# Performance work log

Hardware: AMD Instinct MI355X
Metric: run time of the kernel (lower is better)

The kernel has to match this reference:

```python
import jax, jax.numpy as jnp
import numpy as np

S_LEN, B, H, V, L = 128, 128, 1024, 32000, 2
H2 = 512  # ceil(H/2)
WSZ = 10
MAXW = 2 * WSZ + 1


def setup_inputs() -> dict:
    key = jax.random.key(0)
    k = jax.random.split(key, 16)
    def n(ki, shape, s=0.02):
        return jax.random.normal(ki, shape, dtype=jnp.float32) * s
    return {
        "source_sentence_length": S_LEN,
        "encoder_output": jax.random.normal(k[0], (S_LEN, B, H), dtype=jnp.float32),
        "word": jax.random.randint(k[1], (1, B), 0, V),
        "h0": jax.random.normal(k[2], (L, B, H), dtype=jnp.float32),
        "c0": jax.random.normal(k[3], (L, B, H), dtype=jnp.float32),
        "embedding": n(k[4], (V, H)),
        "lstm_Wih": n(k[5], (L, 4 * H, H)),
        "lstm_Whh": n(k[6], (L, 4 * H, H)),
        "lstm_bih": jnp.zeros((L, 4 * H), jnp.float32),
        "lstm_bhh": jnp.zeros((L, 4 * H), jnp.float32),
        "attn_w1": n(k[7], (H2, H)),
        "attn_b1": jnp.zeros((H2,), jnp.float32),
        "attn_w2": n(k[8], (1, H2)),
        "attn_b2": jnp.zeros((1,), jnp.float32),
        "fc1_w": n(k[9], (H, 2 * H)),
        "fc1_b": jnp.zeros((H,), jnp.float32),
        "fc2_w": n(k[10], (V, H)),
        "fc2_b": jnp.zeros((V,), jnp.float32),
    }


def reference(source_sentence_length, encoder_output, word, h0, c0, embedding,
              lstm_Wih, lstm_Whh, lstm_bih, lstm_bhh,
              attn_w1, attn_b1, attn_w2, attn_b2,
              fc1_w, fc1_b, fc2_w, fc2_b):
    S = source_sentence_length
    std2 = (WSZ / 2.0) ** 2  # std_squared from the module

    # embedding lookup: word [1,B] -> [1,B,H]; single-step multi-layer LSTM
    x = embedding[word][0]  # [B,H]
    hs, cs = [], []
    for l in range(h0.shape[0]):
        gates = x @ lstm_Wih[l].T + lstm_bih[l] + h0[l] @ lstm_Whh[l].T + lstm_bhh[l]
        i, f, g, o = jnp.split(gates, 4, axis=-1)
        c = jax.nn.sigmoid(f) * c0[l] + jax.nn.sigmoid(i) * jnp.tanh(g)
        h = jax.nn.sigmoid(o) * jnp.tanh(c)
        hs.append(h); cs.append(c); x = h
    h_new = jnp.stack(hs)
    c_new = jnp.stack(cs)
    out = x[None]  # decoder output [1,B,H]

    # predicted window center p in [0,S]
    p = S * jax.nn.sigmoid(jnp.tanh(out @ attn_w1.T + attn_b1) @ attn_w2.T + attn_b2)
    pb = p[0, :, 0]  # [B]
    ws = jnp.round(jnp.clip(pb - WSZ, 0, None)).astype(jnp.int32)
    we = jnp.round(jnp.clip(pb + WSZ, None, S - 1)).astype(jnp.int32)

    # windowed gather: position j of window b is source index ws[b]+j
    idx = ws[:, None] + jnp.arange(MAXW, dtype=jnp.int32)  # [B,MAXW]
    valid = idx <= we[:, None]
    enc_b = encoder_output.transpose(1, 0, 2)  # [B,S,H]
    h_s = jnp.take_along_axis(enc_b, jnp.clip(idx, 0, S - 1)[:, :, None], axis=1)
    h_s = jnp.where(valid[:, :, None], h_s, 0.0)  # zero-padded as in the torch code

    # faithful (non-negative, non-squared) gaussian term: exp((pos - p)/(2*std^2))
    gauss = jnp.where(valid, jnp.exp((idx.astype(enc_b.dtype) - pb[:, None]) / (2.0 * std2)), 0.0)

    scores = jnp.einsum('bh,bwh->bw', out[0], h_s)  # zero-padded slots score 0, kept in softmax
    a = jax.nn.softmax(scores, axis=-1) * gauss  # [B,MAXW]
    ctx = jnp.einsum('bw,bwh->bh', a, h_s)[None]  # [1,B,H]

    cat = jnp.concatenate([ctx, out], axis=2)  # [1,B,2H]
    o2 = jnp.tanh(cat @ fc1_w.T + fc1_b)
    y = jax.nn.log_softmax(o2 @ fc2_w.T + fc2_b, axis=2)  # [1,B,V]
    return (y, o2, h_new, c_new, a)
```

## Files before the change

### kernel.cpp

```cpp
#include <hip/hip_runtime.h>
#include <math.h>

namespace {

constexpr int B    = 128;
constexpr int H    = 1024;
constexpr int V    = 32000;
constexpr int WSZ  = 10;
constexpr int MAXW = 2 * WSZ + 1;

typedef __attribute__((ext_vector_type(8))) short bf16x8;
typedef __attribute__((ext_vector_type(4))) short short4v;
typedef __attribute__((ext_vector_type(4))) float f32x4;

__device__ __forceinline__ float sigf(float x) { return 1.0f / (1.0f + expf(-x)); }

__device__ __forceinline__ unsigned short rnebf(float f) {
    unsigned u = __float_as_uint(f);
    u += 0x7fffu + ((u >> 16) & 1u);
    return (unsigned short)(u >> 16);
}

__device__ __forceinline__ bf16x8 cvt8(const f32x4 a, const f32x4 b) {
    bf16x8 r;
    r[0] = (short)rnebf(a.x); r[1] = (short)rnebf(a.y);
    r[2] = (short)rnebf(a.z); r[3] = (short)rnebf(a.w);
    r[4] = (short)rnebf(b.x); r[5] = (short)rnebf(b.y);
    r[6] = (short)rnebf(b.z); r[7] = (short)rnebf(b.w);
    return r;
}

__device__ __forceinline__ void gl_lds16(const float* g, float* l) {
    __builtin_amdgcn_global_load_lds(
        (const __attribute__((address_space(1))) unsigned int*)g,
        (__attribute__((address_space(3))) unsigned int*)l,
        16, 0, 0);
}

struct S3 { short h, m, l; };

__device__ __forceinline__ S3 split3(float x) {
    S3 r;
    const unsigned uh = __float_as_uint(x) & 0xFFFF0000u;
    const float fh = __uint_as_float(uh);
    const float r1 = x - fh;
    const unsigned um = __float_as_uint(r1) & 0xFFFF0000u;
    const float fm = __uint_as_float(um);
    const float r2 = r1 - fm;
    const unsigned ul = __float_as_uint(r2) & 0xFFFF0000u;
    r.h = (short)(uh >> 16);
    r.m = (short)(um >> 16);
    r.l = (short)(ul >> 16);
    return r;
}

__device__ __forceinline__ void split8(const f32x4 a, const f32x4 b,
                                       bf16x8& wh, bf16x8& wm, bf16x8& wl) {
    S3 s;
    s = split3(a.x); wh[0] = s.h; wm[0] = s.m; wl[0] = s.l;
    s = split3(a.y); wh[1] = s.h; wm[1] = s.m; wl[1] = s.l;
    s = split3(a.z); wh[2] = s.h; wm[2] = s.m; wl[2] = s.l;
    s = split3(a.w); wh[3] = s.h; wm[3] = s.m; wl[3] = s.l;
    s = split3(b.x); wh[4] = s.h; wm[4] = s.m; wl[4] = s.l;
    s = split3(b.y); wh[5] = s.h; wm[5] = s.m; wl[5] = s.l;
    s = split3(b.z); wh[6] = s.h; wm[6] = s.m; wl[6] = s.l;
    s = split3(b.w); wh[7] = s.h; wm[7] = s.m; wl[7] = s.l;
}

__global__ __launch_bounds__(256, 2) void lstm_gemm(
    const short* __restrict__ Ah0, const short* __restrict__ Am0, const short* __restrict__ Al0,
    const short* __restrict__ Ah1, const short* __restrict__ Am1, const short* __restrict__ Al1,
    const float* __restrict__ W0, const float* __restrict__ W1,
    float* __restrict__ outbase)
{
    __shared__ float wt[2][4160];

    const int t    = threadIdx.x;
    const int lane = t & 63;
    const int w    = t >> 6;
    const int m16  = lane & 15;
    const int g    = lane >> 4;
    const int n0   = blockIdx.x * 64;
    const int y    = blockIdx.y;
    const int src  = y >> 2;
    const int k0   = (y & 3) * 256;
    const short* Ah = src ? Ah1 : Ah0;
    const short* Am = src ? Am1 : Am0;
    const short* Al = src ? Al1 : Al0;
    const float* W  = src ? W1  : W0;
    float* out = outbase + (size_t)y * 128 * 4096;

    bf16x8 ah[2][8], am[2][8], al[2][8];
    #pragma unroll
    for (int q = 0; q < 2; ++q) {
        const size_t ao = (size_t)((w * 2 + q) * 16 + m16) * 1024 + k0 + g * 8;
        #pragma unroll
        for (int s = 0; s < 8; ++s) {
            ah[q][s] = *(const bf16x8*)(Ah + ao + s * 32);
            am[q][s] = *(const bf16x8*)(Am + ao + s * 32);
            al[q][s] = *(const bf16x8*)(Al + ao + s * 32);
        }
    }

#define LSTM_STAGE(BUF, C)                                                  \
    {                                                                       \
        _Pragma("unroll")                                                   \
        for (int i = 0; i < 5; ++i) {                                       \
            const int idx = i * 256 + t;                                    \
            const int rr  = idx / 65;                                       \
            const int pp  = idx - rr * 65;                                  \
            if (idx < 1040 && pp < 64) {                                    \
                const float* s_ = W + (size_t)(n0 + (C) * 16 + rr) * 1024   \
                                + k0 + pp * 4;                              \
                gl_lds16(s_, &wt[BUF][(size_t)(i * 256 + w * 64) * 4]);     \
            }                                                               \
        }                                                                   \
    }

    LSTM_STAGE(0, 0)
    int cur = 0;
    #pragma unroll
    for (int c = 0; c < 4; ++c) {
        __syncthreads();
        if (c < 3) {
            if (cur == 0) LSTM_STAGE(1, c + 1)
            else          LSTM_STAGE(0, c + 1)
        }
        f32x4 acc0 = {}, acc1 = {};
        const float* lrow = &wt[cur][m16 * 260 + g * 8];
        #pragma unroll
        for (int s = 0; s < 8; ++s) {
            const f32x4 wa = *(const f32x4*)(lrow + s * 32);
            const f32x4 wb = *(const f32x4*)(lrow + s * 32 + 4);
            bf16x8 wh, wm, wl;
            split8(wa, wb, wh, wm, wl);
            acc0 = __builtin_amdgcn_mfma_f32_16x16x32_bf16(ah[0][s], wh, acc0, 0, 0, 0);
            acc0 = __builtin_amdgcn_mfma_f32_16x16x32_bf16(ah[0][s], wm, acc0, 0, 0, 0);
            acc0 = __builtin_amdgcn_mfma_f32_16x16x32_bf16(am[0][s], wh, acc0, 0, 0, 0);
            acc0 = __builtin_amdgcn_mfma_f32_16x16x32_bf16(ah[0][s], wl, acc0, 0, 0, 0);
            acc0 = __builtin_amdgcn_mfma_f32_16x16x32_bf16(am[0][s], wm, acc0, 0, 0, 0);
            acc0 = __builtin_amdgcn_mfma_f32_16x16x32_bf16(al[0][s], wh, acc0, 0, 0, 0);
            acc1 = __builtin_amdgcn_mfma_f32_16x16x32_bf16(ah[1][s], wh, acc1, 0, 0, 0);
            acc1 = __builtin_amdgcn_mfma_f32_16x16x32_bf16(ah[1][s], wm, acc1, 0, 0, 0);
            acc1 = __builtin_amdgcn_mfma_f32_16x16x32_bf16(am[1][s], wh, acc1, 0, 0, 0);
            acc1 = __builtin_amdgcn_mfma_f32_16x16x32_bf16(ah[1][s], wl, acc1, 0, 0, 0);
            acc1 = __builtin_amdgcn_mfma_f32_16x16x32_bf16(am[1][s], wm, acc1, 0, 0, 0);
            acc1 = __builtin_amdgcn_mfma_f32_16x16x32_bf16(al[1][s], wh, acc1, 0, 0, 0);
        }
        const int col = n0 + c * 16 + m16;
        #pragma unroll
        for (int j = 0; j < 4; ++j) {
            out[(size_t)(w * 32 + g * 4 + j) * 4096 + col]      = acc0[j];
            out[(size_t)(w * 32 + 16 + g * 4 + j) * 4096 + col] = acc1[j];
        }
        cur ^= 1;
    }
#undef LSTM_STAGE
}

__global__ __launch_bounds__(256) void fc2_gemm(
    const short* __restrict__ A, const float* __restrict__ W,
    float* __restrict__ outbase)
{
    __shared__ float wt[2][16 * 516];

    const int t    = threadIdx.x;
    const int lane = t & 63;
    const int w    = t >> 6;
    const int m16  = lane & 15;
    const int g    = lane >> 4;
    const int n0   = blockIdx.x * 64;
    const int y    = blockIdx.y;
    const int k0   = y * 512;
    float* out = outbase + (size_t)y * B * V;

    bf16x8 a[2][16];
    #pragma unroll
    for (int q = 0; q < 2; ++q) {
        const short* ap = A + (size_t)((w * 2 + q) * 16 + m16) * 1024 + k0 + g * 8;
        #pragma unroll
        for (int s = 0; s < 16; ++s)
            a[q][s] = *(const bf16x8*)(ap + s * 32);
    }

#define FC2_STAGE(BUF, C)                                                   \
    {                                                                       \
        _Pragma("unroll")                                                   \
        for (int i = 0; i < 9; ++i) {                                       \
            const int idx = i * 256 + t;                                    \
            const int rr  = idx / 129;                                      \
            const int pp  = idx - rr * 129;                                 \
            if (idx < 2064 && pp < 128) {                                   \
                const float* src = W + (size_t)(n0 + (C) * 16 + rr) * 1024  \
                                 + k0 + pp * 4;                             \
                gl_lds16(src, &wt[BUF][(size_t)(i * 256 + w * 64) * 4]);    \
            }                                                               \
        }                                                                   \
    }

    FC2_STAGE(0, 0)
    int cur = 0;
    #pragma unroll
    for (int c = 0; c < 4; ++c) {
        __syncthreads();
        if (c < 3) {
            if (cur == 0) FC2_STAGE(1, c + 1)
            else          FC2_STAGE(0, c + 1)
        }
        f32x4 acc0 = {}, acc1 = {};
        const float* lrow = &wt[cur][m16 * 516 + g * 8];
        #pragma unroll
        for (int s = 0; s < 16; ++s) {
            const f32x4 wa = *(const f32x4*)(lrow + s * 32);
            const f32x4 wb = *(const f32x4*)(lrow + s * 32 + 4);
            const bf16x8 bfr = cvt8(wa, wb);
            acc0 = __builtin_amdgcn_mfma_f32_16x16x32_bf16(a[0][s], bfr, acc0, 0, 0, 0);
            acc1 = __builtin_amdgcn_mfma_f32_16x16x32_bf16(a[1][s], bfr, acc1, 0, 0, 0);
        }
        const int col = n0 + c * 16 + m16;
        #pragma unroll
        for (int j = 0; j < 4; ++j) {
            out[(size_t)(w * 32 + g * 4 + j) * V + col]      = acc0[j];
            out[(size_t)(w * 32 + 16 + g * 4 + j) * V + col] = acc1[j];
        }
        cur ^= 1;
    }
#undef FC2_STAGE
}

__global__ __launch_bounds__(256, 2) void gemm_x3(
    const short* __restrict__ Ah0, const short* __restrict__ Am0, const short* __restrict__ Al0,
    const short* __restrict__ Ah1, const short* __restrict__ Am1, const short* __restrict__ Al1,
    const float* __restrict__ W0, const float* __restrict__ W1,
    int N, int Ksz, int ks_log2, float* __restrict__ outbase)
{
    const int y = blockIdx.y;
    const int src = y >> ks_log2;
    const short* Ah = src ? Ah1 : Ah0;
    const short* Am = src ? Am1 : Am0;
    const short* Al = src ? Al1 : Al0;
    const float* W  = src ? W1  : W0;
    const int k0 = (y & ((1 << ks_log2) - 1)) * Ksz;
    float* out = outbase + (size_t)y * 128 * N;

    const int t    = threadIdx.x;
    const int lane = t & 63;
    const int wv   = t >> 6;
    const int n0   = blockIdx.x * 64 + wv * 16;
    const int m16  = lane & 15;
    const int ko8  = (lane >> 4) * 8;

    const float* wp = W + (size_t)(n0 + m16) * 1024 + k0 + ko8;
    const size_t a0 = (size_t)m16 * 1024 + k0 + ko8;

    f32x4 acc[8] = {};

    f32x4 cwa = *(const f32x4*)(wp);      f32x4 cwb = *(const f32x4*)(wp + 4);
    f32x4 nwa = *(const f32x4*)(wp + 32); f32x4 nwb = *(const f32x4*)(wp + 36);

    for (int kc = 0; kc + 64 < Ksz; kc += 32) {
        bf16x8 ah[8], am[8], al[8];
        #pragma unroll
        for (int m = 0; m < 8; ++m) {
            const size_t ao = a0 + (size_t)m * 16384 + kc;
            ah[m] = *(const bf16x8*)(Ah + ao);
            am[m] = *(const bf16x8*)(Am + ao);
            al[m] = *(const bf16x8*)(Al + ao);
        }
        __builtin_amdgcn_sched_barrier(0);
        const f32x4 fwa = *(const f32x4*)(wp + kc + 64);
        const f32x4 fwb = *(const f32x4*)(wp + kc + 68);
        bf16x8 wh, wm, wl;
        split8(cwa, cwb, wh, wm, wl);
        #pragma unroll
        for (int m = 0; m < 8; ++m) {
            acc[m] = __builtin_amdgcn_mfma_f32_16x16x32_bf16(ah[m], wh, acc[m], 0, 0, 0);
            acc[m] = __builtin_amdgcn_mfma_f32_16x16x32_bf16(ah[m], wm, acc[m], 0, 0, 0);
            acc[m] = __builtin_amdgcn_mfma_f32_16x16x32_bf16(am[m], wh, acc[m], 0, 0, 0);
            acc[m] = __builtin_amdgcn_mfma_f32_16x16x32_bf16(ah[m], wl, acc[m], 0, 0, 0);
            acc[m] = __builtin_amdgcn_mfma_f32_16x16x32_bf16(am[m], wm, acc[m], 0, 0, 0);
            acc[m] = __builtin_amdgcn_mfma_f32_16x16x32_bf16(al[m], wh, acc[m], 0, 0, 0);
        }
        cwa = nwa; cwb = nwb; nwa = fwa; nwb = fwb;
    }
    #pragma unroll
    for (int tail = 0; tail < 2; ++tail) {
        const int kc = Ksz - 64 + tail * 32;
        bf16x8 ah[8], am[8], al[8];
        #pragma unroll
        for (int m = 0; m < 8; ++m) {
            const size_t ao = a0 + (size_t)m * 16384 + kc;
            ah[m] = *(const bf16x8*)(Ah + ao);
            am[m] = *(const bf16x8*)(Am + ao);
            al[m] = *(const bf16x8*)(Al + ao);
        }
        const f32x4 wa = tail ? nwa : cwa;
        const f32x4 wb = tail ? nwb : cwb;
        bf16x8 wh, wm, wl;
        split8(wa, wb, wh, wm, wl);
        #pragma unroll
        for (int m = 0; m < 8; ++m) {
            acc[m] = __builtin_amdgcn_mfma_f32_16x16x32_bf16(ah[m], wh, acc[m], 0, 0, 0);
            acc[m] = __builtin_amdgcn_mfma_f32_16x16x32_bf16(ah[m], wm, acc[m], 0, 0, 0);
            acc[m] = __builtin_amdgcn_mfma_f32_16x16x32_bf16(am[m], wh, acc[m], 0, 0, 0);
            acc[m] = __builtin_amdgcn_mfma_f32_16x16x32_bf16(ah[m], wl, acc[m], 0, 0, 0);
            acc[m] = __builtin_amdgcn_mfma_f32_16x16x32_bf16(am[m], wm, acc[m], 0, 0, 0);
            acc[m] = __builtin_amdgcn_mfma_f32_16x16x32_bf16(al[m], wh, acc[m], 0, 0, 0);
        }
    }

    #pragma unroll
    for (int m = 0; m < 8; ++m) {
        const int rbase = m * 16 + (lane >> 4) * 4;
        #pragma unroll
        for (int r = 0; r < 4; ++r)
            out[(size_t)(rbase + r) * N + n0 + m16] = acc[m][r];
    }
}

__global__ __launch_bounds__(256) void fc1_gemm(
    const short* __restrict__ A0, const short* __restrict__ A1,
    const float* __restrict__ W, float* __restrict__ outbase)
{
    const int y = blockIdx.y;
    const int src = y >> 3;
    const short* A = src ? A1 : A0;
    const int k0 = (y & 7) * 128;
    const int wk0 = src * 1024 + k0;
    float* out = outbase + (size_t)y * 128 * 1024;

    const int t    = threadIdx.x;
    const int lane = t & 63;
    const int wv   = t >> 6;
    const int n0   = blockIdx.x * 64 + wv * 16;
    const int m16  = lane & 15;
    const int ko8  = (lane >> 4) * 8;

    const float* wp = W + (size_t)(n0 + m16) * 2048 + wk0 + ko8;
    const short* ap = A + (size_t)m16 * 1024 + k0 + ko8;

    f32x4 acc[8] = {};

    #pragma unroll
    for (int kc = 0; kc < 128; kc += 32) {
        bf16x8 afr[8];
        #pragma unroll
        for (int m = 0; m < 8; ++m)
            afr[m] = *(const bf16x8*)(ap + (size_t)m * 16384 + kc);
        const f32x4 wa = *(const f32x4*)(wp + kc);
        const f32x4 wb = *(const f32x4*)(wp + kc + 4);
        const bf16x8 bfr = cvt8(wa, wb);
        #pragma unroll
        for (int m = 0; m < 8; ++m)
            acc[m] = __builtin_amdgcn_mfma_f32_16x16x32_bf16(afr[m], bfr, acc[m], 0, 0, 0);
    }

    #pragma unroll
    for (int m = 0; m < 8; ++m) {
        const int rbase = m * 16 + (lane >> 4) * 4;
        #pragma unroll
        for (int r = 0; r < 4; ++r)
            out[(size_t)(rbase + r) * 1024 + n0 + m16] = acc[m][r];
    }
}

__global__ void prep_k(const int* __restrict__ word, const float* __restrict__ emb,
                       const float* __restrict__ h0,
                       short* __restrict__ xh, short* __restrict__ xm, short* __restrict__ xl,
                       short* __restrict__ h0h, short* __restrict__ h0m, short* __restrict__ h0l)
{
    const int blk = blockIdx.x, t = threadIdx.x;
    const float* src; short *dh, *dm, *dl; size_t off;
    if (blk < 128) {
        src = emb + (size_t)word[blk] * H; off = (size_t)blk * H;
        dh = xh; dm = xm; dl = xl;
    } else {
        const int i = blk - 128;
        src = h0 + (size_t)i * H; off = (size_t)i * H;
        dh = h0h; dm = h0m; dl = h0l;
    }
    const float4 v = ((const float4*)src)[t];
    short4v sh, sm, sl;
    S3 s;
    s = split3(v.x); sh.x = s.h; sm.x = s.m; sl.x = s.l;
    s = split3(v.y); sh.y = s.h; sm.y = s.m; sl.y = s.l;
    s = split3(v.z); sh.z = s.h; sm.z = s.m; sl.z = s.l;
    s = split3(v.w); sh.w = s.h; sm.w = s.m; sl.w = s.l;
    *(short4v*)(dh + off + t * 4) = sh;
    *(short4v*)(dm + off + t * 4) = sm;
    *(short4v*)(dl + off + t * 4) = sl;
}

__global__ void lstm_cell_k(const float* __restrict__ part,
                            const float* __restrict__ bih, const float* __restrict__ bhh,
                            const float* __restrict__ c0,
                            float* __restrict__ h_out, float* __restrict__ c_out,
                            short* __restrict__ xh, short* __restrict__ xm,
                            short* __restrict__ xl)
{
    const int idx = blockIdx.x * 256 + threadIdx.x;
    const int b = idx >> 10, hh = idx & 1023;
    const size_t base = (size_t)b * 4096;
    float g[4];
    #pragma unroll
    for (int j = 0; j < 4; ++j) {
        const int o = hh + j * H;
        float s = bih[o] + bhh[o];
        #pragma unroll
        for (int i = 0; i < 8; ++i) s += part[base + o + (size_t)i * 524288];
        g[j] = s;
    }
    const float c = sigf(g[1]) * c0[idx] + sigf(g[0]) * tanhf(g[2]);
    const float h = sigf(g[3]) * tanhf(c);
    c_out[idx] = c;
    h_out[idx] = h;
    const S3 s = split3(h);
    xh[idx] = s.h; xm[idx] = s.m; xl[idx] = s.l;
}

__global__ void attn_ctx_k(const float* __restrict__ part, const float* __restrict__ b1,
                           const float* __restrict__ w2v, const float* __restrict__ b2,
                           const int* __restrict__ Sptr,
                           const float* __restrict__ x, const float* __restrict__ enc,
                           float* __restrict__ a_out, short* __restrict__ ctxb)
{
    __shared__ float red[256];
    __shared__ float so[H];
    __shared__ float swred[4][MAXW];
    __shared__ float ssc[MAXW];
    __shared__ float sa[MAXW];
    __shared__ float sp;
    __shared__ int sw0, sw1;
    const int b = blockIdx.x, t = threadIdx.x;
    const int lane = t & 63, wvv = t >> 6;

    {
        const float* pa = part + (size_t)b * 512;
        float v = 0.f;
        #pragma unroll
        for (int jj = 0; jj < 2; ++jj) {
            const int j = t + jj * 256;
            float sgm = b1[j];
            #pragma unroll
            for (int i = 0; i < 16; ++i) sgm += pa[j + (size_t)i * 65536];
            v += tanhf(sgm) * w2v[j];
        }
        red[t] = v;
        __syncthreads();
        for (int s = 128; s > 0; s >>= 1) {
            if (t < s) red[t] += red[t + s];
            __syncthreads();
        }
        if (t == 0) {
            const float S = (float)Sptr[0];
            const float sv = S * sigf(red[0] + b2[0]);
            sp  = sv;
            sw0 = (int)rintf(fmaxf(sv - (float)WSZ, 0.f));
            sw1 = (int)rintf(fminf(sv + (float)WSZ, S - 1.f));
        }
    }
    for (int h = t; h < H; h += 256) so[h] = x[(size_t)b * H + h];
    __syncthreads();
    const int w0 = sw0, w1e = sw1;
    const float pbv = sp;

    float ps[MAXW];
    #pragma unroll
    for (int w = 0; w < MAXW; ++w) ps[w] = 0.f;
    for (int h4 = t; h4 < H / 4; h4 += 256) {
        const float4 o = ((const float4*)so)[h4];
        #pragma unroll
        for (int w = 0; w < MAXW; ++w) {
            const int idx = w0 + w;
            if (idx <= w1e) {
                const float4 e = *(const float4*)(enc + ((size_t)idx * B + b) * H + h4 * 4);
                ps[w] += o.x * e.x + o.y * e.y + o.z * e.z + o.w * e.w;
            }
        }
    }
    #pragma unroll
    for (int w = 0; w < MAXW; ++w) {
        float v = ps[w];
        for (int off = 32; off > 0; off >>= 1) v += __shfl_down(v, off);
        if (lane == 0) swred[wvv][w] = v;
    }
    __syncthreads();
    if (t == 0) {
        float m = -1e30f;
        for (int w = 0; w < MAXW; ++w) {
            const float s = swred[0][w] + swred[1][w] + swred[2][w] + swred[3][w];
            ssc[w] = s;
            m = fmaxf(m, s);
        }
        float den = 0.f;
        for (int w = 0; w < MAXW; ++w) den += expf(ssc[w] - m);
        for (int w = 0; w < MAXW; ++w) {
            const int idx = w0 + w;
            const float gauss = (idx <= w1e) ? expf(((float)idx - pbv) / 50.0f) : 0.f;
            sa[w] = expf(ssc[w] - m) / den * gauss;
        }
    }
    __syncthreads();
    if (t < MAXW) a_out[b * MAXW + t] = sa[t];
    for (int h4 = t; h4 < H / 4; h4 += 256) {
        float4 acc = {0.f, 0.f, 0.f, 0.f};
        #pragma unroll
        for (int w = 0; w < MAXW; ++w) {
            const int idx = w0 + w;
            if (idx <= w1e) {
                const float4 e = *(const float4*)(enc + ((size_t)idx * B + b) * H + h4 * 4);
                acc.x += sa[w] * e.x; acc.y += sa[w] * e.y;
                acc.z += sa[w] * e.z; acc.w += sa[w] * e.w;
            }
        }
        short4v s;
        s.x = (short)rnebf(acc.x); s.y = (short)rnebf(acc.y);
        s.z = (short)rnebf(acc.z); s.w = (short)rnebf(acc.w);
        *(short4v*)(ctxb + (size_t)b * H + h4 * 4) = s;
    }
}

__global__ void fc1_fin_k(const float* __restrict__ part, const float* __restrict__ bias,
                          float* __restrict__ o2, short* __restrict__ o2b)
{
    const int idx = blockIdx.x * 256 + threadIdx.x;
    const int n = idx & 1023;
    float v = bias[n];
    #pragma unroll
    for (int i = 0; i < 16; ++i) v += part[idx + (size_t)i * 131072];
    v = tanhf(v);
    o2[idx] = v;
    o2b[idx] = (short)rnebf(v);
}

__global__ __launch_bounds__(1024) void lsm_k(
    const float* __restrict__ p0, const float* __restrict__ p1,
    const float* __restrict__ bias, float* __restrict__ y)
{
    __shared__ float sm[16], ss[16], slse;
    const int b = blockIdx.x, t = threadIdx.x;
    const float* r0 = p0 + (size_t)b * V;
    const float* r1 = p1 + (size_t)b * V;
    float* yrow = y + (size_t)b * V;

    f32x4 r[8];
    float m = -1e30f, s = 0.f;
    #pragma unroll
    for (int i = 0; i < 8; ++i) {
        const int v4 = t + i * 1024;
        if (v4 < V / 4) {
            const f32x4 a = ((const f32x4*)r0)[v4];
            const f32x4 c = ((const f32x4*)r1)[v4];
            const f32x4 bv = ((const f32x4*)bias)[v4];
            f32x4 q;
            q.x = a.x + c.x + bv.x; q.y = a.y + c.y + bv.y;
            q.z = a.z + c.z + bv.z; q.w = a.w + c.w + bv.w;
            r[i] = q;
            const float mm = fmaxf(fmaxf(q.x, q.y), fmaxf(q.z, q.w));
            if (mm > m) { s *= expf(m - mm); m = mm; }
            s += expf(q.x - m) + expf(q.y - m) + expf(q.z - m) + expf(q.w - m);
        }
    }
    for (int off = 32; off > 0; off >>= 1) {
        const float mo = __shfl_down(m, off), so = __shfl_down(s, off);
        const float mn = fmaxf(m, mo);
        s = s * expf(m - mn) + so * expf(mo - mn);
        m = mn;
    }
    const int wv = t >> 6, lane = t & 63;
    if (lane == 0) { sm[wv] = m; ss[wv] = s; }
    __syncthreads();
    if (t == 0) {
        float M = sm[0], S = ss[0];
        for (int i = 1; i < 16; ++i) {
            const float mn = fmaxf(M, sm[i]);
            S = S * expf(M - mn) + ss[i] * expf(sm[i] - mn);
            M = mn;
        }
        slse = M + logf(S);
    }
    __syncthreads();
    const float lse = slse;
    #pragma unroll
    for (int i = 0; i < 8; ++i) {
        const int v4 = t + i * 1024;
        if (v4 < V / 4) {
            f32x4 q = r[i];
            q.x -= lse; q.y -= lse; q.z -= lse; q.w -= lse;
            ((f32x4*)yrow)[v4] = q;
        }
    }
}

}

extern "C" void kernel_launch(void* const* d_in, const int* in_sizes, int n_in,
                              void* d_out, int out_size, void* d_ws, size_t ws_size,
                              hipStream_t stream)
{
    const int*   Sp   = (const int*)d_in[0];
    const float* enc  = (const float*)d_in[1];
    const int*   word = (const int*)d_in[2];
    const float* h0   = (const float*)d_in[3];
    const float* c0   = (const float*)d_in[4];
    const float* emb  = (const float*)d_in[5];
    const float* Wih  = (const float*)d_in[6];
    const float* Whh  = (const float*)d_in[7];
    const float* bih  = (const float*)d_in[8];
    const float* bhh  = (const float*)d_in[9];
    const float* aw1  = (const float*)d_in[10];
    const float* ab1  = (const float*)d_in[11];
    const float* aw2  = (const float*)d_in[12];
    const float* ab2  = (const float*)d_in[13];
    const float* f1w  = (const float*)d_in[14];
    const float* f1b  = (const float*)d_in[15];
    const float* f2w  = (const float*)d_in[16];
    const float* f2b  = (const float*)d_in[17];

    float* outp = (float*)d_out;
    float* y    = outp;
    float* o2   = y  + (size_t)B * V;
    float* hN   = o2 + (size_t)B * H;
    float* cN   = hN + 2 * (size_t)B * H;
    float* aO   = cN + 2 * (size_t)B * H;

    char* wsp = (char*)d_ws;
    short* xh   = (short*)wsp;  wsp += (size_t)B * H * 2;
    short* xm   = (short*)wsp;  wsp += (size_t)B * H * 2;
    short* xl   = (short*)wsp;  wsp += (size_t)B * H * 2;
    short* h0h  = (short*)wsp;  wsp += (size_t)2 * B * H * 2;
    short* h0m  = (short*)wsp;  wsp += (size_t)2 * B * H * 2;
    short* h0l  = (short*)wsp;  wsp += (size_t)2 * B * H * 2;
    short* ctxb = (short*)wsp;  wsp += (size_t)B * H * 2;
    short* o2b  = (short*)wsp;  wsp += (size_t)B * H * 2;
    float* part = (float*)wsp;  wsp += (size_t)16 * B * 4 * H * 4;
    float* pf2  = (float*)wsp;  wsp += (size_t)2 * B * V * 4;

    prep_k<<<dim3(384), dim3(256), 0, stream>>>(word, emb, h0, xh, xm, xl, h0h, h0m, h0l);

    for (int l = 0; l < 2; ++l) {
        lstm_gemm<<<dim3(64, 8), dim3(256), 0, stream>>>(
            xh, xm, xl,
            h0h + (size_t)l * B * H, h0m + (size_t)l * B * H, h0l + (size_t)l * B * H,
            Wih + (size_t)l * 4 * H * H, Whh + (size_t)l * 4 * H * H,
            part);
        lstm_cell_k<<<dim3(B * H / 256), dim3(256), 0, stream>>>(
            part, bih + (size_t)l * 4 * H, bhh + (size_t)l * 4 * H,
            c0 + (size_t)l * B * H,
            hN + (size_t)l * B * H, cN + (size_t)l * B * H, xh, xm, xl);
    }

    const float* hfin = hN + (size_t)B * H;

    gemm_x3<<<dim3(8, 16), dim3(256), 0, stream>>>(
        xh, xm, xl, xh, xm, xl, aw1, aw1, 512, 64, 4, part);
    attn_ctx_k<<<dim3(B), dim3(256), 0, stream>>>(
        part, ab1, aw2, ab2, Sp, hfin, enc, aO, ctxb);

    fc1_gemm<<<dim3(16, 16), dim3(256), 0, stream>>>(ctxb, xh, f1w, part);
    fc1_fin_k<<<dim3(B * H / 256), dim3(256), 0, stream>>>(part, f1b, o2, o2b);

    fc2_gemm<<<dim3(V / 64, 2), dim3(256), 0, stream>>>(o2b, f2w, pf2);

    lsm_k<<<dim3(B), dim3(1024), 0, stream>>>(pf2, pf2 + (size_t)B * V, f2b, y);
}
```

Measured before the change: 170.7 us.

## Drop fc2 split-K partials and restructure fc1 with LDS-staged weights

Result: slower. 200.5 us (+17.4%).

```diff
diff --git a/kernel.cpp b/kernel.cpp
--- a/kernel.cpp
+++ b/kernel.cpp
@@ -158,9 +158,9 @@
 #undef LSTM_STAGE
 }
 
-__global__ __launch_bounds__(256) void fc2_gemm(
+__global__ __launch_bounds__(256, 2) void fc2_gemm(
     const short* __restrict__ A, const float* __restrict__ W,
-    float* __restrict__ outbase)
+    const float* __restrict__ bias, float* __restrict__ out)
 {
     __shared__ float wt[2][16 * 516];
 
@@ -170,16 +170,13 @@
     const int m16  = lane & 15;
     const int g    = lane >> 4;
     const int n0   = blockIdx.x * 64;
-    const int y    = blockIdx.y;
-    const int k0   = y * 512;
-    float* out = outbase + (size_t)y * B * V;
-
-    bf16x8 a[2][16];
+
+    bf16x8 a[2][32];
     #pragma unroll
     for (int q = 0; q < 2; ++q) {
-        const short* ap = A + (size_t)((w * 2 + q) * 16 + m16) * 1024 + k0 + g * 8;
-        #pragma unroll
-        for (int s = 0; s < 16; ++s)
+        const short* ap = A + (size_t)((w * 2 + q) * 16 + m16) * 1024 + g * 8;
+        #pragma unroll
+        for (int s = 0; s < 32; ++s)
             a[q][s] = *(const bf16x8*)(ap + s * 32);
     }
 
@@ -191,8 +188,9 @@
             const int rr  = idx / 129;                                      \
             const int pp  = idx - rr * 129;                                 \
             if (idx < 2064 && pp < 128) {                                   \
-                const float* src = W + (size_t)(n0 + (C) * 16 + rr) * 1024  \
-                                 + k0 + pp * 4;                             \
+                const float* src = W                                        \
+                    + (size_t)(n0 + ((C) >> 1) * 16 + rr) * 1024            \
+                    + ((C) & 1) * 512 + pp * 4;                             \
                 gl_lds16(src, &wt[BUF][(size_t)(i * 256 + w * 64) * 4]);    \
             }                                                               \
         }                                                                   \
@@ -200,28 +198,33 @@
 
     FC2_STAGE(0, 0)
     int cur = 0;
-    #pragma unroll
-    for (int c = 0; c < 4; ++c) {
+    f32x4 acc0 = {}, acc1 = {};
+    #pragma unroll
+    for (int c = 0; c < 8; ++c) {
         __syncthreads();
-        if (c < 3) {
+        if (c < 7) {
             if (cur == 0) FC2_STAGE(1, c + 1)
             else          FC2_STAGE(0, c + 1)
         }
-        f32x4 acc0 = {}, acc1 = {};
+        if ((c & 1) == 0) { acc0 = {}; acc1 = {}; }
         const float* lrow = &wt[cur][m16 * 516 + g * 8];
         #pragma unroll
         for (int s = 0; s < 16; ++s) {
             const f32x4 wa = *(const f32x4*)(lrow + s * 32);
             const f32x4 wb = *(const f32x4*)(lrow + s * 32 + 4);
             const bf16x8 bfr = cvt8(wa, wb);
-            acc0 = __builtin_amdgcn_mfma_f32_16x16x32_bf16(a[0][s], bfr, acc0, 0, 0, 0);
-            acc1 = __builtin_amdgcn_mfma_f32_16x16x32_bf16(a[1][s], bfr, acc1, 0, 0, 0);
-        }
-        const int col = n0 + c * 16 + m16;
-        #pragma unroll
-        for (int j = 0; j < 4; ++j) {
-            out[(size_t)(w * 32 + g * 4 + j) * V + col]      = acc0[j];
-            out[(size_t)(w * 32 + 16 + g * 4 + j) * V + col] = acc1[j];
+            const int ks = (c & 1) * 16 + s;
+            acc0 = __builtin_amdgcn_mfma_f32_16x16x32_bf16(a[0][ks], bfr, acc0, 0, 0, 0);
+            acc1 = __builtin_amdgcn_mfma_f32_16x16x32_bf16(a[1][ks], bfr, acc1, 0, 0, 0);
+        }
+        if (c & 1) {
+            const int col = n0 + (c >> 1) * 16 + m16;
+            const float bv = bias[col];
+            #pragma unroll
+            for (int j = 0; j < 4; ++j) {
+                out[(size_t)(w * 32 + g * 4 + j) * V + col]      = acc0[j] + bv;
+                out[(size_t)(w * 32 + 16 + g * 4 + j) * V + col] = acc1[j] + bv;
+            }
         }
         cur ^= 1;
     }
@@ -318,50 +321,77 @@
     }
 }
 
-__global__ __launch_bounds__(256) void fc1_gemm(
+__global__ __launch_bounds__(256, 2) void fc1_gemm(
     const short* __restrict__ A0, const short* __restrict__ A1,
     const float* __restrict__ W, float* __restrict__ outbase)
 {
-    const int y = blockIdx.y;
-    const int src = y >> 3;
-    const short* A = src ? A1 : A0;
-    const int k0 = (y & 7) * 128;
-    const int wk0 = src * 1024 + k0;
-    float* out = outbase + (size_t)y * 128 * 1024;
+    __shared__ float wt[2][16 * 132];
 
     const int t    = threadIdx.x;
     const int lane = t & 63;
-    const int wv   = t >> 6;
-    const int n0   = blockIdx.x * 64 + wv * 16;
+    const int w    = t >> 6;
     const int m16  = lane & 15;
-    const int ko8  = (lane >> 4) * 8;
-
-    const float* wp = W + (size_t)(n0 + m16) * 2048 + wk0 + ko8;
-    const short* ap = A + (size_t)m16 * 1024 + k0 + ko8;
-
-    f32x4 acc[8] = {};
-
-    #pragma unroll
-    for (int kc = 0; kc < 128; kc += 32) {
-        bf16x8 afr[8];
-        #pragma unroll
-        for (int m = 0; m < 8; ++m)
-            afr[m] = *(const bf16x8*)(ap + (size_t)m * 16384 + kc);
-        const f32x4 wa = *(const f32x4*)(wp + kc);
-        const f32x4 wb = *(const f32x4*)(wp + kc + 4);
-        const bf16x8 bfr = cvt8(wa, wb);
-        #pragma unroll
-        for (int m = 0; m < 8; ++m)
-            acc[m] = __builtin_amdgcn_mfma_f32_16x16x32_bf16(afr[m], bfr, acc[m], 0, 0, 0);
-    }
-
-    #pragma unroll
-    for (int m = 0; m < 8; ++m) {
-        const int rbase = m * 16 + (lane >> 4) * 4;
-        #pragma unroll
-        for (int r = 0; r < 4; ++r)
-            out[(size_t)(rbase + r) * 1024 + n0 + m16] = acc[m][r];
-    }
+    const int g    = lane >> 4;
+    const int n0   = blockIdx.x * 64;
+    const int y    = blockIdx.y;
+    const int src  = y >> 3;
+    const int k0   = (y & 7) * 128;
+    const int wk0  = src * 1024 + k0;
+    const short* A = src ? A1 : A0;
+    float* out = outbase + (size_t)y * 128 * 1024;
+
+    bf16x8 a[2][4];
+    #pragma unroll
+    for (int q = 0; q < 2; ++q) {
+        const short* ap = A + (size_t)((w * 2 + q) * 16 + m16) * 1024 + k0 + g * 8;
+        #pragma unroll
+        for (int s = 0; s < 4; ++s)
+            a[q][s] = *(const bf16x8*)(ap + s * 32);
+    }
+
+#define FC1_STAGE(BUF, C)                                                   \
+    {                                                                       \
+        _Pragma("unroll")                                                   \
+        for (int i = 0; i < 3; ++i) {                                       \
+            const int idx = i * 256 + t;                                    \
+            const int rr  = idx / 33;                                       \
+            const int pp  = idx - rr * 33;                                  \
+            if (idx < 528 && pp < 32) {                                     \
+                const float* s_ = W + (size_t)(n0 + (C) * 16 + rr) * 2048   \
+                                + wk0 + pp * 4;                             \
+                gl_lds16(s_, &wt[BUF][(size_t)(i * 256 + w * 64) * 4]);     \
+            }                                                               \
+        }                                                                   \
+    }
+
+    FC1_STAGE(0, 0)
+    int cur = 0;
+    #pragma unroll
+    for (int c = 0; c < 4; ++c) {
+        __syncthreads();
+        if (c < 3) {
+            if (cur == 0) FC1_STAGE(1, c + 1)
+            else          FC1_STAGE(0, c + 1)
+        }
+        f32x4 acc0 = {}, acc1 = {};
+        const float* lrow = &wt[cur][m16 * 132 + g * 8];
+        #pragma unroll
+        for (int s = 0; s < 4; ++s) {
+            const f32x4 wa = *(const f32x4*)(lrow + s * 32);
+            const f32x4 wb = *(const f32x4*)(lrow + s * 32 + 4);
+            const bf16x8 bfr = cvt8(wa, wb);
+            acc0 = __builtin_amdgcn_mfma_f32_16x16x32_bf16(a[0][s], bfr, acc0, 0, 0, 0);
+            acc1 = __builtin_amdgcn_mfma_f32_16x16x32_bf16(a[1][s], bfr, acc1, 0, 0, 0);
+        }
+        const int col = n0 + c * 16 + m16;
+        #pragma unroll
+        for (int j = 0; j < 4; ++j) {
+            out[(size_t)(w * 32 + g * 4 + j) * 1024 + col]      = acc0[j];
+            out[(size_t)(w * 32 + 16 + g * 4 + j) * 1024 + col] = acc1[j];
+        }
+        cur ^= 1;
+    }
+#undef FC1_STAGE
 }
 
 __global__ void prep_k(const int* __restrict__ word, const float* __restrict__ emb,
@@ -533,14 +563,10 @@
     o2b[idx] = (short)rnebf(v);
 }
 
-__global__ __launch_bounds__(1024) void lsm_k(
-    const float* __restrict__ p0, const float* __restrict__ p1,
-    const float* __restrict__ bias, float* __restrict__ y)
+__global__ __launch_bounds__(1024) void lsm_k(float* __restrict__ y)
 {
     __shared__ float sm[16], ss[16], slse;
     const int b = blockIdx.x, t = threadIdx.x;
-    const float* r0 = p0 + (size_t)b * V;
-    const float* r1 = p1 + (size_t)b * V;
     float* yrow = y + (size_t)b * V;
 
     f32x4 r[8];
@@ -549,12 +575,7 @@
     for (int i = 0; i < 8; ++i) {
         const int v4 = t + i * 1024;
         if (v4 < V / 4) {
-            const f32x4 a = ((const f32x4*)r0)[v4];
-            const f32x4 c = ((const f32x4*)r1)[v4];
-            const f32x4 bv = ((const f32x4*)bias)[v4];
-            f32x4 q;
-            q.x = a.x + c.x + bv.x; q.y = a.y + c.y + bv.y;
-            q.z = a.z + c.z + bv.z; q.w = a.w + c.w + bv.w;
+            const f32x4 q = ((const f32x4*)yrow)[v4];
             r[i] = q;
             const float mm = fmaxf(fmaxf(q.x, q.y), fmaxf(q.z, q.w));
             if (mm > m) { s *= expf(m - mm); m = mm; }
@@ -634,7 +655,6 @@
     short* ctxb = (short*)wsp;  wsp += (size_t)B * H * 2;
     short* o2b  = (short*)wsp;  wsp += (size_t)B * H * 2;
     float* part = (float*)wsp;  wsp += (size_t)16 * B * 4 * H * 4;
-    float* pf2  = (float*)wsp;  wsp += (size_t)2 * B * V * 4;
 
     prep_k<<<dim3(384), dim3(256), 0, stream>>>(word, emb, h0, xh, xm, xl, h0h, h0m, h0l);
 
@@ -660,7 +680,7 @@
     fc1_gemm<<<dim3(16, 16), dim3(256), 0, stream>>>(ctxb, xh, f1w, part);
     fc1_fin_k<<<dim3(B * H / 256), dim3(256), 0, stream>>>(part, f1b, o2, o2b);
 
-    fc2_gemm<<<dim3(V / 64, 2), dim3(256), 0, stream>>>(o2b, f2w, pf2);
-
-    lsm_k<<<dim3(B), dim3(1024), 0, stream>>>(pf2, pf2 + (size_t)B * V, f2b, y);
-}
+    fc2_gemm<<<dim3(V / 64), dim3(256), 0, stream>>>(o2b, f2w, f2b, y);
+
+    lsm_k<<<dim3(B), dim3(1024), 0, stream>>>(y);
+}
```
